# Kernel tuning notes

Hardware: AMD Instinct MI355X
Metric: run time of the kernel (lower is better)

Reference implementation:

```python
import jax, jax.numpy as jnp
import numpy as np

CH = 256
DQK = CH // 8


def setup_inputs() -> dict:
    key = jax.random.key(0)
    ks = jax.random.split(key, 8)
    B, C, H, W = 4, CH, 64, 64
    x = jax.random.normal(ks[0], (B, C, H, W), dtype=jnp.float32)
    s = 1.0 / np.sqrt(C)
    Wq = jax.random.normal(ks[1], (DQK, C), dtype=jnp.float32) * s
    bq = jnp.zeros((DQK,), dtype=jnp.float32)
    Wk = jax.random.normal(ks[2], (DQK, C), dtype=jnp.float32) * s
    bk = jnp.zeros((DQK,), dtype=jnp.float32)
    Wv = jax.random.normal(ks[3], (C, C), dtype=jnp.float32) * s
    bv = jnp.zeros((C,), dtype=jnp.float32)
    gamma = jnp.zeros((1,), dtype=jnp.float32)
    return {"x": x, "Wq": Wq, "bq": bq, "Wk": Wk, "bk": bk, "Wv": Wv, "bv": bv, "gamma": gamma}


def reference(x, Wq, bq, Wk, bk, Wv, bv, gamma):
    B, C, H, W = x.shape
    N = H * W
    xf = x.reshape(B, C, N)                                   # [B, C, N]
    # 1x1 convs == per-position linear maps over channels
    q = jnp.einsum('dc,bcn->bdn', Wq, xf) + bq[None, :, None]  # [B, D, N]
    k = jnp.einsum('dc,bcn->bdn', Wk, xf) + bk[None, :, None]  # [B, D, N]
    v = jnp.einsum('oc,bcn->bon', Wv, xf) + bv[None, :, None]  # [B, C, N]
    # energy[b,i,j] = <q[:, i], k[:, j]>  (no 1/sqrt(d) scaling, as in source)
    energy = jnp.einsum('bdi,bdj->bij', q, k)                  # [B, N, N]
    attn = jax.nn.softmax(energy, axis=-1)                     # softmax over j
    # out[b,c,i] = sum_j v[b,c,j] * attn[b,i,j]
    out = jnp.einsum('bcj,bij->bci', v, attn)                  # [B, C, N]
    return x + gamma[0] * out.reshape(B, C, H, W)
```

## Files before the change

kernel.cpp:

```cpp
#include <hip/hip_runtime.h>
#include <hip/hip_bf16.h>

#define NB   4
#define NC   256
#define NPOS 4096
#define NDQK 32

typedef __bf16 bf16x8  __attribute__((ext_vector_type(8)));
typedef float  f32x16  __attribute__((ext_vector_type(16)));
typedef unsigned int u32x4 __attribute__((ext_vector_type(4)));


__global__ __launch_bounds__(256) void proj_kernel(
    const float* __restrict__ x,
    const float* __restrict__ Wq, const float* __restrict__ bq,
    const float* __restrict__ Wk, const float* __restrict__ bk,
    const float* __restrict__ Wv, const float* __restrict__ bv,
    __hip_bfloat16* __restrict__ Qb, __hip_bfloat16* __restrict__ Kb,
    __hip_bfloat16* __restrict__ Vb)
{
    const int t   = threadIdx.x;
    const int l   = t & 63;
    const int w   = t >> 6;
    const int hi  = l >> 5;
    const int col = l & 31;
    const int row = l & 31;

    const int item = blockIdx.x * 4 + w;
    const int th   = item & 1;
    const int nch  = (item >> 1) & 63;
    const int rest = item >> 7;
    const int g    = rest % 5;
    const int b    = rest / 5;

    const float *W0, *W1, *bs0, *bs1;
    int o0 = 0, o1 = 0;
    if (g < 4) {
        o0 = g * 64; o1 = g * 64 + 32;
        W0 = Wv + (size_t)o0 * NC; W1 = Wv + (size_t)o1 * NC;
        bs0 = bv + o0; bs1 = bv + o1;
    } else {
        W0 = Wq; W1 = Wk; bs0 = bq; bs1 = bk;
    }

    bf16x8 wf0[16], wf1[16];
    const float* Wr0 = W0 + (size_t)row * NC + 8 * hi;
    const float* Wr1 = W1 + (size_t)row * NC + 8 * hi;
    #pragma unroll
    for (int kk = 0; kk < 16; ++kk) {
        float4 a0 = *reinterpret_cast<const float4*>(Wr0 + kk * 16);
        float4 c0 = *reinterpret_cast<const float4*>(Wr0 + kk * 16 + 4);
        float4 a1 = *reinterpret_cast<const float4*>(Wr1 + kk * 16);
        float4 c1 = *reinterpret_cast<const float4*>(Wr1 + kk * 16 + 4);
        bf16x8 f0, f1;
        f0[0] = (__bf16)a0.x; f0[1] = (__bf16)a0.y; f0[2] = (__bf16)a0.z; f0[3] = (__bf16)a0.w;
        f0[4] = (__bf16)c0.x; f0[5] = (__bf16)c0.y; f0[6] = (__bf16)c0.z; f0[7] = (__bf16)c0.w;
        f1[0] = (__bf16)a1.x; f1[1] = (__bf16)a1.y; f1[2] = (__bf16)a1.z; f1[3] = (__bf16)a1.w;
        f1[4] = (__bf16)c1.x; f1[5] = (__bf16)c1.y; f1[6] = (__bf16)c1.z; f1[7] = (__bf16)c1.w;
        wf0[kk] = f0; wf1[kk] = f1;
    }

    const int n0 = nch * 64 + th * 32;
    f32x16 acc0, acc1;
    #pragma unroll
    for (int r = 0; r < 16; ++r) { acc0[r] = 0.f; acc1[r] = 0.f; }

    const float* xcol = x + (size_t)b * NC * NPOS + n0 + col;
    #pragma unroll
    for (int kk = 0; kk < 16; ++kk) {
        bf16x8 bf;
        #pragma unroll
        for (int i = 0; i < 8; ++i)
            bf[i] = (__bf16)xcol[(size_t)(kk * 16 + 8 * hi + i) * NPOS];
        acc0 = __builtin_amdgcn_mfma_f32_32x32x16_bf16(wf0[kk], bf, acc0, 0, 0, 0);
        acc1 = __builtin_amdgcn_mfma_f32_32x32x16_bf16(wf1[kk], bf, acc1, 0, 0, 0);
    }

    if (g < 4) {
        __hip_bfloat16* vt = Vb + (size_t)b * NC * NPOS
                                + (size_t)(n0 >> 5) * 8192 + (size_t)g * 2048
                                + ((col >> 4) << 9) + (((col >> 3) & 1) << 8)
                                + (col & 7);
        #pragma unroll
        for (int r = 0; r < 16; ++r) {
            const int orow = (r & 3) + 8 * (r >> 2) + 4 * hi;
            vt[orow * 8]        = __float2bfloat16(acc0[r] + bs0[orow]);
            vt[1024 + orow * 8] = __float2bfloat16(acc1[r] + bs1[orow]);
        }
    } else {
        #pragma unroll
        for (int r = 0; r < 16; ++r) {
            const int orow = (r & 3) + 8 * (r >> 2) + 4 * hi;
            const size_t nidx = (size_t)(b * NPOS) + n0 + col;
            Qb[nidx * NDQK + orow] =
                __float2bfloat16((acc0[r] + bs0[orow]) * 1.44269504088896f);
            Kb[nidx * NDQK + orow] =
                __float2bfloat16(acc1[r] + bs1[orow]);
        }
    }
}

__global__ __launch_bounds__(512, 2) void attn_kernel(
    const __hip_bfloat16* __restrict__ Qb,
    const __hip_bfloat16* __restrict__ Kb,
    const __hip_bfloat16* __restrict__ Vb,
    const float* __restrict__ x,
    const float* __restrict__ gamma,
    float* __restrict__ out)
{
    __shared__ float olds[NC * 64];
    __shared__ float lsum[64];
    const int t   = threadIdx.x;
    const int l   = t & 63;
    const int w   = t >> 6;
    const int cg  = w & 3;
    const int jh  = w >> 2;
    const int hi  = l >> 5;
    const int q   = l & 31;
    const int bx  = blockIdx.x;
    const int b   = (bx >> 1) & 3;
    const int qt  = ((bx >> 3) << 1) | (bx & 1);
    const int q0  = qt * 64;
    const int c0w = cg * 64;

    const __bf16* Qp = reinterpret_cast<const __bf16*>(Qb) + (size_t)b * NPOS * NDQK;
    const __bf16* Kp = reinterpret_cast<const __bf16*>(Kb) + (size_t)b * NPOS * NDQK;
    const __bf16* Vp = reinterpret_cast<const __bf16*>(Vb) + (size_t)b * NC * NPOS;

    const int perm = (q & 0x13) | ((q & 4) << 1) | ((q & 8) >> 1);

    const bf16x8 qf00 = *reinterpret_cast<const bf16x8*>(Qp + (size_t)(q0 + q) * NDQK + 8 * hi);
    const bf16x8 qf01 = *reinterpret_cast<const bf16x8*>(Qp + (size_t)(q0 + q) * NDQK + 16 + 8 * hi);
    const bf16x8 qf10 = *reinterpret_cast<const bf16x8*>(Qp + (size_t)(q0 + 32 + q) * NDQK + 8 * hi);
    const bf16x8 qf11 = *reinterpret_cast<const bf16x8*>(Qp + (size_t)(q0 + 32 + q) * NDQK + 16 + 8 * hi);

    const int jt0 = jh * 64;
    const __bf16* kp = Kp + (size_t)perm * NDQK + 8 * hi + (size_t)jt0 * 1024;
    const __bf16* vp = Vp + (size_t)cg * 2048 + l * 8 + (size_t)jt0 * 8192;

    #define LOADT(k0, k1, v0, v1, v2, v3, kptr, vptr)                      \
        asm volatile(                                                      \
            "global_load_dwordx4 %0, %6, off\n\t"                          \
            "global_load_dwordx4 %1, %6, off offset:32\n\t"                \
            "global_load_dwordx4 %2, %7, off\n\t"                          \
            "global_load_dwordx4 %3, %7, off offset:1024\n\t"              \
            "global_load_dwordx4 %4, %7, off offset:2048\n\t"              \
            "global_load_dwordx4 %5, %7, off offset:3072"                  \
            : "=&v"(k0), "=&v"(k1), "=&v"(v0), "=&v"(v1), "=&v"(v2), "=&v"(v3) \
            : "v"(kptr), "v"(vptr)                                         \
            : "memory")

    f32x16 acc00, acc01, acc10, acc11;
    #pragma unroll
    for (int r = 0; r < 16; ++r) { acc00[r] = 0.f; acc01[r] = 0.f; acc10[r] = 0.f; acc11[r] = 0.f; }
    float lp0 = 0.f, lp1 = 0.f;

    f32x16 z16;
    #pragma unroll
    for (int r = 0; r < 16; ++r) z16[r] = 0.f;

    auto compute = [&](u32x4 k0r, u32x4 k1r, u32x4 v0r, u32x4 v1r,
                       u32x4 v2r, u32x4 v3r) {
        const bf16x8 kc0 = __builtin_bit_cast(bf16x8, k0r);
        const bf16x8 kc1 = __builtin_bit_cast(bf16x8, k1r);
        const bf16x8 vc0 = __builtin_bit_cast(bf16x8, v0r);
        const bf16x8 vc1 = __builtin_bit_cast(bf16x8, v1r);
        const bf16x8 vc2 = __builtin_bit_cast(bf16x8, v2r);
        const bf16x8 vc3 = __builtin_bit_cast(bf16x8, v3r);

        f32x16 s0 = __builtin_amdgcn_mfma_f32_32x32x16_bf16(kc0, qf00, z16, 0, 0, 0);
        s0 = __builtin_amdgcn_mfma_f32_32x32x16_bf16(kc1, qf01, s0, 0, 0, 0);
        f32x16 s1 = __builtin_amdgcn_mfma_f32_32x32x16_bf16(kc0, qf10, z16, 0, 0, 0);
        s1 = __builtin_amdgcn_mfma_f32_32x32x16_bf16(kc1, qf11, s1, 0, 0, 0);

        float p0[16], p1[16];
        #pragma unroll
        for (int r = 0; r < 16; ++r) p0[r] = __builtin_amdgcn_exp2f(s0[r]);
        #pragma unroll
        for (int r = 0; r < 16; ++r) p1[r] = __builtin_amdgcn_exp2f(s1[r]);

        lp0 += (((p0[0] + p0[1]) + (p0[2] + p0[3])) + ((p0[4] + p0[5]) + (p0[6] + p0[7])))
             + (((p0[8] + p0[9]) + (p0[10] + p0[11])) + ((p0[12] + p0[13]) + (p0[14] + p0[15])));
        lp1 += (((p1[0] + p1[1]) + (p1[2] + p1[3])) + ((p1[4] + p1[5]) + (p1[6] + p1[7])))
             + (((p1[8] + p1[9]) + (p1[10] + p1[11])) + ((p1[12] + p1[13]) + (p1[14] + p1[15])));

        bf16x8 pa00, pa01, pa10, pa11;
        #pragma unroll
        for (int i = 0; i < 8; ++i) {
            pa00[i] = (__bf16)p0[i]; pa01[i] = (__bf16)p0[8 + i];
            pa10[i] = (__bf16)p1[i]; pa11[i] = (__bf16)p1[8 + i];
        }

        acc00 = __builtin_amdgcn_mfma_f32_32x32x16_bf16(vc0, pa00, acc00, 0, 0, 0);
        acc00 = __builtin_amdgcn_mfma_f32_32x32x16_bf16(vc1, pa01, acc00, 0, 0, 0);
        acc01 = __builtin_amdgcn_mfma_f32_32x32x16_bf16(vc2, pa00, acc01, 0, 0, 0);
        acc01 = __builtin_amdgcn_mfma_f32_32x32x16_bf16(vc3, pa01, acc01, 0, 0, 0);
        acc10 = __builtin_amdgcn_mfma_f32_32x32x16_bf16(vc0, pa10, acc10, 0, 0, 0);
        acc10 = __builtin_amdgcn_mfma_f32_32x32x16_bf16(vc1, pa11, acc10, 0, 0, 0);
        acc11 = __builtin_amdgcn_mfma_f32_32x32x16_bf16(vc2, pa10, acc11, 0, 0, 0);
        acc11 = __builtin_amdgcn_mfma_f32_32x32x16_bf16(vc3, pa11, acc11, 0, 0, 0);
    };

    u32x4 ka0, ka1, va0, va1, va2, va3;
    u32x4 kb0, kb1, vb0, vb1, vb2, vb3;

    LOADT(ka0, ka1, va0, va1, va2, va3, kp, vp);
    kp += 1024; vp += 8192;
    asm volatile("s_waitcnt vmcnt(0)" ::: "memory");
    __builtin_amdgcn_sched_barrier(0);

    #pragma unroll 1
    for (int i = 0; i < 64; i += 2) {
        LOADT(kb0, kb1, vb0, vb1, vb2, vb3, kp, vp);
        __builtin_amdgcn_sched_barrier(0);
        if (i < 62) { kp += 1024; vp += 8192; }
        compute(ka0, ka1, va0, va1, va2, va3);
        asm volatile("s_waitcnt vmcnt(0)" ::: "memory");
        __builtin_amdgcn_sched_barrier(0);

        LOADT(ka0, ka1, va0, va1, va2, va3, kp, vp);
        __builtin_amdgcn_sched_barrier(0);
        if (i < 60) { kp += 1024; vp += 8192; }
        compute(kb0, kb1, vb0, vb1, vb2, vb3);
        asm volatile("s_waitcnt vmcnt(0)" ::: "memory");
        __builtin_amdgcn_sched_barrier(0);
    }
    #undef LOADT

    const float lt0 = lp0 + __shfl_xor(lp0, 32);
    const float lt1 = lp1 + __shfl_xor(lp1, 32);

    if (jh == 0) {
        #pragma unroll
        for (int r = 0; r < 16; ++r) {
            const int crow = (r & 3) + 8 * (r >> 2) + 4 * hi;
            olds[(c0w + crow) * 64 + q]           = acc00[r];
            olds[(c0w + 32 + crow) * 64 + q]      = acc01[r];
            olds[(c0w + crow) * 64 + 32 + q]      = acc10[r];
            olds[(c0w + 32 + crow) * 64 + 32 + q] = acc11[r];
        }
        if (cg == 0) { lsum[q + 32 * hi] = hi ? lt1 : lt0; }
    }
    __syncthreads();
    if (jh == 1) {
        const float gm  = gamma[0];
        const float gl0 = gm / (lt0 + lsum[q]);
        const float gl1 = gm / (lt1 + lsum[32 + q]);
        #pragma unroll
        for (int r = 0; r < 16; ++r) {
            const int crow = (r & 3) + 8 * (r >> 2) + 4 * hi;
            const size_t g00 = ((size_t)(b * NC + c0w + crow)) * NPOS + q0 + q;
            const size_t g01 = g00 + (size_t)32 * NPOS;
            out[g00]      = x[g00]      + gl0 * (acc00[r] + olds[(c0w + crow) * 64 + q]);
            out[g01]      = x[g01]      + gl0 * (acc01[r] + olds[(c0w + 32 + crow) * 64 + q]);
            out[g00 + 32] = x[g00 + 32] + gl1 * (acc10[r] + olds[(c0w + crow) * 64 + 32 + q]);
            out[g01 + 32] = x[g01 + 32] + gl1 * (acc11[r] + olds[(c0w + 32 + crow) * 64 + 32 + q]);
        }
    }
}

extern "C" void kernel_launch(void* const* d_in, const int* in_sizes, int n_in,
                              void* d_out, int out_size, void* d_ws, size_t ws_size,
                              hipStream_t stream) {
    (void)in_sizes; (void)n_in; (void)out_size; (void)ws_size;
    const float* x     = (const float*)d_in[0];
    const float* Wq    = (const float*)d_in[1];
    const float* bq    = (const float*)d_in[2];
    const float* Wk    = (const float*)d_in[3];
    const float* bk    = (const float*)d_in[4];
    const float* Wv    = (const float*)d_in[5];
    const float* bv    = (const float*)d_in[6];
    const float* gamma = (const float*)d_in[7];
    float* out = (float*)d_out;

    char* ws = (char*)d_ws;
    __hip_bfloat16* Qb = (__hip_bfloat16*)(ws);
    __hip_bfloat16* Kb = (__hip_bfloat16*)(ws + (1u << 20));
    __hip_bfloat16* Vb = (__hip_bfloat16*)(ws + (2u << 20));

    proj_kernel<<<640, 256, 0, stream>>>(x, Wq, bq, Wk, bk, Wv, bv, Qb, Kb, Vb);
    attn_kernel<<<256, 512, 0, stream>>>(Qb, Kb, Vb, x, gamma, out);
}
```

Baseline: 96.87 us.

## Split attention blocks by channel group and reduce four key quarters in LDS

Measured after the change: 96.38 us. Within noise of the previous version (-0.5%).

```diff
diff --git a/kernel.cpp b/kernel.cpp
--- a/kernel.cpp
+++ b/kernel.cpp
@@ -100,7 +100,7 @@
     }
 }
 
-__global__ __launch_bounds__(512, 2) void attn_kernel(
+__global__ __launch_bounds__(256, 2) void attn_kernel(
     const __hip_bfloat16* __restrict__ Qb,
     const __hip_bfloat16* __restrict__ Kb,
     const __hip_bfloat16* __restrict__ Vb,
@@ -108,20 +108,20 @@
     const float* __restrict__ gamma,
     float* __restrict__ out)
 {
-    __shared__ float olds[NC * 64];
-    __shared__ float lsum[64];
+    __shared__ float olds[2 * 64 * 64];
+    __shared__ float lsum[4 * 64];
     const int t   = threadIdx.x;
     const int l   = t & 63;
-    const int w   = t >> 6;
-    const int cg  = w & 3;
-    const int jh  = w >> 2;
+    const int jq  = t >> 6;
     const int hi  = l >> 5;
     const int q   = l & 31;
     const int bx  = blockIdx.x;
     const int b   = (bx >> 1) & 3;
-    const int qt  = ((bx >> 3) << 1) | (bx & 1);
+    const int id  = ((bx >> 3) << 1) | (bx & 1);
+    const int qt  = id >> 2;
+    const int cg  = id & 3;
     const int q0  = qt * 64;
-    const int c0w = cg * 64;
+    const int c0  = cg * 64;
 
     const __bf16* Qp = reinterpret_cast<const __bf16*>(Qb) + (size_t)b * NPOS * NDQK;
     const __bf16* Kp = reinterpret_cast<const __bf16*>(Kb) + (size_t)b * NPOS * NDQK;
@@ -134,7 +134,7 @@
     const bf16x8 qf10 = *reinterpret_cast<const bf16x8*>(Qp + (size_t)(q0 + 32 + q) * NDQK + 8 * hi);
     const bf16x8 qf11 = *reinterpret_cast<const bf16x8*>(Qp + (size_t)(q0 + 32 + q) * NDQK + 16 + 8 * hi);
 
-    const int jt0 = jh * 64;
+    const int jt0 = jq * 32;
     const __bf16* kp = Kp + (size_t)perm * NDQK + 8 * hi + (size_t)jt0 * 1024;
     const __bf16* vp = Vp + (size_t)cg * 2048 + l * 8 + (size_t)jt0 * 8192;
 
@@ -210,17 +210,17 @@
     __builtin_amdgcn_sched_barrier(0);
 
     #pragma unroll 1
-    for (int i = 0; i < 64; i += 2) {
+    for (int i = 0; i < 32; i += 2) {
         LOADT(kb0, kb1, vb0, vb1, vb2, vb3, kp, vp);
         __builtin_amdgcn_sched_barrier(0);
-        if (i < 62) { kp += 1024; vp += 8192; }
+        if (i < 30) { kp += 1024; vp += 8192; }
         compute(ka0, ka1, va0, va1, va2, va3);
         asm volatile("s_waitcnt vmcnt(0)" ::: "memory");
         __builtin_amdgcn_sched_barrier(0);
 
         LOADT(ka0, ka1, va0, va1, va2, va3, kp, vp);
         __builtin_amdgcn_sched_barrier(0);
-        if (i < 60) { kp += 1024; vp += 8192; }
+        if (i < 30) { kp += 1024; vp += 8192; }
         compute(kb0, kb1, vb0, vb1, vb2, vb3);
         asm volatile("s_waitcnt vmcnt(0)" ::: "memory");
         __builtin_amdgcn_sched_barrier(0);
@@ -230,31 +230,41 @@
     const float lt0 = lp0 + __shfl_xor(lp0, 32);
     const float lt1 = lp1 + __shfl_xor(lp1, 32);
 
-    if (jh == 0) {
+    lsum[jq * 64 + 32 * hi + q] = hi ? lt1 : lt0;
+
+    float* buf = olds + (jq & 1) * 4096;
+    if (jq < 2) {
         #pragma unroll
         for (int r = 0; r < 16; ++r) {
             const int crow = (r & 3) + 8 * (r >> 2) + 4 * hi;
-            olds[(c0w + crow) * 64 + q]           = acc00[r];
-            olds[(c0w + 32 + crow) * 64 + q]      = acc01[r];
-            olds[(c0w + crow) * 64 + 32 + q]      = acc10[r];
-            olds[(c0w + 32 + crow) * 64 + 32 + q] = acc11[r];
-        }
-        if (cg == 0) { lsum[q + 32 * hi] = hi ? lt1 : lt0; }
+            buf[(crow) * 64 + q]           = acc00[r];
+            buf[(32 + crow) * 64 + q]      = acc01[r];
+            buf[(crow) * 64 + 32 + q]      = acc10[r];
+            buf[(32 + crow) * 64 + 32 + q] = acc11[r];
+        }
     }
     __syncthreads();
-    if (jh == 1) {
-        const float gm  = gamma[0];
-        const float gl0 = gm / (lt0 + lsum[q]);
-        const float gl1 = gm / (lt1 + lsum[32 + q]);
+    if (jq >= 2) {
         #pragma unroll
         for (int r = 0; r < 16; ++r) {
             const int crow = (r & 3) + 8 * (r >> 2) + 4 * hi;
-            const size_t g00 = ((size_t)(b * NC + c0w + crow)) * NPOS + q0 + q;
-            const size_t g01 = g00 + (size_t)32 * NPOS;
-            out[g00]      = x[g00]      + gl0 * (acc00[r] + olds[(c0w + crow) * 64 + q]);
-            out[g01]      = x[g01]      + gl0 * (acc01[r] + olds[(c0w + 32 + crow) * 64 + q]);
-            out[g00 + 32] = x[g00 + 32] + gl1 * (acc10[r] + olds[(c0w + crow) * 64 + 32 + q]);
-            out[g01 + 32] = x[g01 + 32] + gl1 * (acc11[r] + olds[(c0w + 32 + crow) * 64 + 32 + q]);
+            buf[(crow) * 64 + q]           += acc00[r];
+            buf[(32 + crow) * 64 + q]      += acc01[r];
+            buf[(crow) * 64 + 32 + q]      += acc10[r];
+            buf[(32 + crow) * 64 + 32 + q] += acc11[r];
+        }
+    }
+    __syncthreads();
+    {
+        const float gm   = gamma[0];
+        const float ltot = lsum[l] + lsum[64 + l] + lsum[128 + l] + lsum[192 + l];
+        const float gl   = gm / ltot;
+        #pragma unroll
+        for (int rr = 0; rr < 16; ++rr) {
+            const int c = jq * 16 + rr;
+            const float v = olds[c * 64 + l] + olds[4096 + c * 64 + l];
+            const size_t gi = ((size_t)(b * NC + c0 + c)) * NPOS + q0 + l;
+            out[gi] = x[gi] + gl * v;
         }
     }
 }
@@ -279,5 +289,5 @@
     __hip_bfloat16* Vb = (__hip_bfloat16*)(ws + (2u << 20));
 
     proj_kernel<<<640, 256, 0, stream>>>(x, Wq, bq, Wk, bk, Wv, bv, Qb, Kb, Vb);
-    attn_kernel<<<256, 512, 0, stream>>>(Qb, Kb, Vb, x, gamma, out);
+    attn_kernel<<<1024, 256, 0, stream>>>(Qb, Kb, Vb, x, gamma, out);
 }
```

## Share QK^T softmax work across waves via LDS and DMA K/V tiles

Applied to the files above, without the earlier changes.

Result: faster. 91.97 us (-5.1%).

```diff
diff --git a/kernel.cpp b/kernel.cpp
--- a/kernel.cpp
+++ b/kernel.cpp
@@ -8,7 +8,9 @@
 
 typedef __bf16 bf16x8  __attribute__((ext_vector_type(8)));
 typedef float  f32x16  __attribute__((ext_vector_type(16)));
-typedef unsigned int u32x4 __attribute__((ext_vector_type(4)));
+
+typedef __attribute__((address_space(3))) char*       lds_ptr_t;
+typedef const __attribute__((address_space(1))) char* glb_ptr_t;
 
 
 __global__ __launch_bounds__(256) void proj_kernel(
@@ -91,16 +93,22 @@
         #pragma unroll
         for (int r = 0; r < 16; ++r) {
             const int orow = (r & 3) + 8 * (r >> 2) + 4 * hi;
-            const size_t nidx = (size_t)(b * NPOS) + n0 + col;
-            Qb[nidx * NDQK + orow] =
+            Qb[((size_t)(b * NPOS) + n0 + col) * NDQK + orow] =
                 __float2bfloat16((acc0[r] + bs0[orow]) * 1.44269504088896f);
-            Kb[nidx * NDQK + orow] =
+        }
+        const int prow = (col & 0x13) | ((col & 4) << 1) | ((col & 8) >> 1);
+        __hip_bfloat16* kt = Kb + (size_t)b * (NPOS * 32)
+                                + (size_t)(n0 >> 5) * 1024 + prow * 8;
+        #pragma unroll
+        for (int r = 0; r < 16; ++r) {
+            const int orow = (r & 3) + 8 * (r >> 2) + 4 * hi;
+            kt[(orow >> 4) * 512 + ((orow >> 3) & 1) * 256 + (orow & 7)] =
                 __float2bfloat16(acc1[r] + bs1[orow]);
         }
     }
 }
 
-__global__ __launch_bounds__(512, 2) void attn_kernel(
+__global__ __launch_bounds__(256, 1) void attn_kernel(
     const __hip_bfloat16* __restrict__ Qb,
     const __hip_bfloat16* __restrict__ Kb,
     const __hip_bfloat16* __restrict__ Vb,
@@ -108,47 +116,47 @@
     const float* __restrict__ gamma,
     float* __restrict__ out)
 {
-    __shared__ float olds[NC * 64];
-    __shared__ float lsum[64];
-    const int t   = threadIdx.x;
-    const int l   = t & 63;
-    const int w   = t >> 6;
-    const int cg  = w & 3;
-    const int jh  = w >> 2;
-    const int hi  = l >> 5;
-    const int q   = l & 31;
-    const int bx  = blockIdx.x;
-    const int b   = (bx >> 1) & 3;
-    const int qt  = ((bx >> 3) << 1) | (bx & 1);
-    const int q0  = qt * 64;
-    const int c0w = cg * 64;
+    __shared__ __align__(16) char smem[8192 + 32768 + 16384 + 1024];
+    const int t  = threadIdx.x;
+    const int l  = t & 63;
+    const int w  = t >> 6;
+    const int hi = l >> 5;
+    const int q  = l & 31;
+    const int bx = blockIdx.x;
+    const int b  = (bx >> 1) & 3;
+    const int qt = ((bx >> 3) << 1) | (bx & 1);
+    const int q0 = qt * 64;
+    const int c0 = w * 64;
 
     const __bf16* Qp = reinterpret_cast<const __bf16*>(Qb) + (size_t)b * NPOS * NDQK;
-    const __bf16* Kp = reinterpret_cast<const __bf16*>(Kb) + (size_t)b * NPOS * NDQK;
+    const __bf16* Kp = reinterpret_cast<const __bf16*>(Kb) + (size_t)b * (NPOS * 32);
     const __bf16* Vp = reinterpret_cast<const __bf16*>(Vb) + (size_t)b * NC * NPOS;
-
-    const int perm = (q & 0x13) | ((q & 4) << 1) | ((q & 8) >> 1);
 
     const bf16x8 qf00 = *reinterpret_cast<const bf16x8*>(Qp + (size_t)(q0 + q) * NDQK + 8 * hi);
     const bf16x8 qf01 = *reinterpret_cast<const bf16x8*>(Qp + (size_t)(q0 + q) * NDQK + 16 + 8 * hi);
     const bf16x8 qf10 = *reinterpret_cast<const bf16x8*>(Qp + (size_t)(q0 + 32 + q) * NDQK + 8 * hi);
     const bf16x8 qf11 = *reinterpret_cast<const bf16x8*>(Qp + (size_t)(q0 + 32 + q) * NDQK + 16 + 8 * hi);
-
-    const int jt0 = jh * 64;
-    const __bf16* kp = Kp + (size_t)perm * NDQK + 8 * hi + (size_t)jt0 * 1024;
-    const __bf16* vp = Vp + (size_t)cg * 2048 + l * 8 + (size_t)jt0 * 8192;
-
-    #define LOADT(k0, k1, v0, v1, v2, v3, kptr, vptr)                      \
-        asm volatile(                                                      \
-            "global_load_dwordx4 %0, %6, off\n\t"                          \
-            "global_load_dwordx4 %1, %6, off offset:32\n\t"                \
-            "global_load_dwordx4 %2, %7, off\n\t"                          \
-            "global_load_dwordx4 %3, %7, off offset:1024\n\t"              \
-            "global_load_dwordx4 %4, %7, off offset:2048\n\t"              \
-            "global_load_dwordx4 %5, %7, off offset:3072"                  \
-            : "=&v"(k0), "=&v"(k1), "=&v"(v0), "=&v"(v1), "=&v"(v2), "=&v"(v3) \
-            : "v"(kptr), "v"(vptr)                                         \
-            : "memory")
+    asm volatile("" :: "v"(qf00), "v"(qf01), "v"(qf10), "v"(qf11));
+
+    char* kb_lds = smem + w * 2048;
+    char* vb_lds = smem + 8192 + w * 8192;
+    __bf16* kbuf = reinterpret_cast<__bf16*>(kb_lds);
+    __bf16* vbuf = reinterpret_cast<__bf16*>(vb_lds);
+    __bf16* plds = reinterpret_cast<__bf16*>(smem + 40960);
+    float*  lsum = reinterpret_cast<float*>(smem + 57344);
+
+    const __bf16* ksrc = Kp + (size_t)w * 1024 + l * 8;
+    const __bf16* vsrc = Vp + (size_t)w * 2048 + l * 8;
+
+    #define DMA16(dst, src) __builtin_amdgcn_global_load_lds( \
+        (glb_ptr_t)(const char*)(src), (lds_ptr_t)(dst), 16, 0, 0)
+    #define DMAK(tp) do { DMA16(kb_lds, (tp)); DMA16(kb_lds + 1024, (tp) + 512); } while (0)
+    #define DMAV(bi, tp) do {                                   \
+        DMA16(vb_lds + (bi) * 4096,        (tp));               \
+        DMA16(vb_lds + (bi) * 4096 + 1024, (tp) + 512);         \
+        DMA16(vb_lds + (bi) * 4096 + 2048, (tp) + 1024);        \
+        DMA16(vb_lds + (bi) * 4096 + 3072, (tp) + 1536);        \
+    } while (0)
 
     f32x16 acc00, acc01, acc10, acc11;
     #pragma unroll
@@ -159,38 +167,16 @@
     #pragma unroll
     for (int r = 0; r < 16; ++r) z16[r] = 0.f;
 
-    auto compute = [&](u32x4 k0r, u32x4 k1r, u32x4 v0r, u32x4 v1r,
-                       u32x4 v2r, u32x4 v3r) {
-        const bf16x8 kc0 = __builtin_bit_cast(bf16x8, k0r);
-        const bf16x8 kc1 = __builtin_bit_cast(bf16x8, k1r);
-        const bf16x8 vc0 = __builtin_bit_cast(bf16x8, v0r);
-        const bf16x8 vc1 = __builtin_bit_cast(bf16x8, v1r);
-        const bf16x8 vc2 = __builtin_bit_cast(bf16x8, v2r);
-        const bf16x8 vc3 = __builtin_bit_cast(bf16x8, v3r);
-
-        f32x16 s0 = __builtin_amdgcn_mfma_f32_32x32x16_bf16(kc0, qf00, z16, 0, 0, 0);
-        s0 = __builtin_amdgcn_mfma_f32_32x32x16_bf16(kc1, qf01, s0, 0, 0, 0);
-        f32x16 s1 = __builtin_amdgcn_mfma_f32_32x32x16_bf16(kc0, qf10, z16, 0, 0, 0);
-        s1 = __builtin_amdgcn_mfma_f32_32x32x16_bf16(kc1, qf11, s1, 0, 0, 0);
-
-        float p0[16], p1[16];
-        #pragma unroll
-        for (int r = 0; r < 16; ++r) p0[r] = __builtin_amdgcn_exp2f(s0[r]);
-        #pragma unroll
-        for (int r = 0; r < 16; ++r) p1[r] = __builtin_amdgcn_exp2f(s1[r]);
-
-        lp0 += (((p0[0] + p0[1]) + (p0[2] + p0[3])) + ((p0[4] + p0[5]) + (p0[6] + p0[7])))
-             + (((p0[8] + p0[9]) + (p0[10] + p0[11])) + ((p0[12] + p0[13]) + (p0[14] + p0[15])));
-        lp1 += (((p1[0] + p1[1]) + (p1[2] + p1[3])) + ((p1[4] + p1[5]) + (p1[6] + p1[7])))
-             + (((p1[8] + p1[9]) + (p1[10] + p1[11])) + ((p1[12] + p1[13]) + (p1[14] + p1[15])));
-
-        bf16x8 pa00, pa01, pa10, pa11;
-        #pragma unroll
-        for (int i = 0; i < 8; ++i) {
-            pa00[i] = (__bf16)p0[i]; pa01[i] = (__bf16)p0[8 + i];
-            pa10[i] = (__bf16)p1[i]; pa11[i] = (__bf16)p1[8 + i];
-        }
-
+    auto PV = [&](int tt, const __bf16* vf) {
+        const bf16x8 vc0 = *reinterpret_cast<const bf16x8*>(vf);
+        const bf16x8 vc1 = *reinterpret_cast<const bf16x8*>(vf + 512);
+        const bf16x8 vc2 = *reinterpret_cast<const bf16x8*>(vf + 1024);
+        const bf16x8 vc3 = *reinterpret_cast<const bf16x8*>(vf + 1536);
+        const __bf16* pf = plds + tt * 2048 + l * 8;
+        const bf16x8 pa00 = *reinterpret_cast<const bf16x8*>(pf);
+        const bf16x8 pa01 = *reinterpret_cast<const bf16x8*>(pf + 512);
+        const bf16x8 pa10 = *reinterpret_cast<const bf16x8*>(pf + 1024);
+        const bf16x8 pa11 = *reinterpret_cast<const bf16x8*>(pf + 1536);
         acc00 = __builtin_amdgcn_mfma_f32_32x32x16_bf16(vc0, pa00, acc00, 0, 0, 0);
         acc00 = __builtin_amdgcn_mfma_f32_32x32x16_bf16(vc1, pa01, acc00, 0, 0, 0);
         acc01 = __builtin_amdgcn_mfma_f32_32x32x16_bf16(vc2, pa00, acc01, 0, 0, 0);
@@ -201,61 +187,106 @@
         acc11 = __builtin_amdgcn_mfma_f32_32x32x16_bf16(vc3, pa11, acc11, 0, 0, 0);
     };
 
-    u32x4 ka0, ka1, va0, va1, va2, va3;
-    u32x4 kb0, kb1, vb0, vb1, vb2, vb3;
-
-    LOADT(ka0, ka1, va0, va1, va2, va3, kp, vp);
-    kp += 1024; vp += 8192;
-    asm volatile("s_waitcnt vmcnt(0)" ::: "memory");
-    __builtin_amdgcn_sched_barrier(0);
+    DMAK(ksrc);
+    DMAV(0, vsrc);
 
     #pragma unroll 1
-    for (int i = 0; i < 64; i += 2) {
-        LOADT(kb0, kb1, vb0, vb1, vb2, vb3, kp, vp);
-        __builtin_amdgcn_sched_barrier(0);
-        if (i < 62) { kp += 1024; vp += 8192; }
-        compute(ka0, ka1, va0, va1, va2, va3);
-        asm volatile("s_waitcnt vmcnt(0)" ::: "memory");
-        __builtin_amdgcn_sched_barrier(0);
-
-        LOADT(ka0, ka1, va0, va1, va2, va3, kp, vp);
-        __builtin_amdgcn_sched_barrier(0);
-        if (i < 60) { kp += 1024; vp += 8192; }
-        compute(kb0, kb1, vb0, vb1, vb2, vb3);
-        asm volatile("s_waitcnt vmcnt(0)" ::: "memory");
-        __builtin_amdgcn_sched_barrier(0);
-    }
-    #undef LOADT
+    for (int r = 0; r < 32; ++r) {
+        asm volatile("s_waitcnt vmcnt(4)" ::: "memory");
+        __builtin_amdgcn_sched_barrier(0);
+        {
+            const bf16x8 kc0 = *reinterpret_cast<const bf16x8*>(kbuf + l * 8);
+            const bf16x8 kc1 = *reinterpret_cast<const bf16x8*>(kbuf + 512 + l * 8);
+            f32x16 s0 = __builtin_amdgcn_mfma_f32_32x32x16_bf16(kc0, qf00, z16, 0, 0, 0);
+            s0 = __builtin_amdgcn_mfma_f32_32x32x16_bf16(kc1, qf01, s0, 0, 0, 0);
+            f32x16 s1 = __builtin_amdgcn_mfma_f32_32x32x16_bf16(kc0, qf10, z16, 0, 0, 0);
+            s1 = __builtin_amdgcn_mfma_f32_32x32x16_bf16(kc1, qf11, s1, 0, 0, 0);
+
+            float p0[16], p1[16];
+            #pragma unroll
+            for (int i = 0; i < 16; ++i) p0[i] = __builtin_amdgcn_exp2f(s0[i]);
+            #pragma unroll
+            for (int i = 0; i < 16; ++i) p1[i] = __builtin_amdgcn_exp2f(s1[i]);
+
+            lp0 += (((p0[0] + p0[1]) + (p0[2] + p0[3])) + ((p0[4] + p0[5]) + (p0[6] + p0[7])))
+                 + (((p0[8] + p0[9]) + (p0[10] + p0[11])) + ((p0[12] + p0[13]) + (p0[14] + p0[15])));
+            lp1 += (((p1[0] + p1[1]) + (p1[2] + p1[3])) + ((p1[4] + p1[5]) + (p1[6] + p1[7])))
+                 + (((p1[8] + p1[9]) + (p1[10] + p1[11])) + ((p1[12] + p1[13]) + (p1[14] + p1[15])));
+
+            bf16x8 pa00, pa01, pa10, pa11;
+            #pragma unroll
+            for (int i = 0; i < 8; ++i) {
+                pa00[i] = (__bf16)p0[i]; pa01[i] = (__bf16)p0[8 + i];
+                pa10[i] = (__bf16)p1[i]; pa11[i] = (__bf16)p1[8 + i];
+            }
+            __bf16* pw = plds + w * 2048 + l * 8;
+            *reinterpret_cast<bf16x8*>(pw)        = pa00;
+            *reinterpret_cast<bf16x8*>(pw + 512)  = pa01;
+            *reinterpret_cast<bf16x8*>(pw + 1024) = pa10;
+            *reinterpret_cast<bf16x8*>(pw + 1536) = pa11;
+        }
+        asm volatile("s_waitcnt lgkmcnt(0)" ::: "memory");
+        __builtin_amdgcn_s_barrier();
+        __builtin_amdgcn_sched_barrier(0);
+
+        DMAV(1, vsrc + 1 * 8192);
+        asm volatile("s_waitcnt vmcnt(4)" ::: "memory");
+        __builtin_amdgcn_sched_barrier(0);
+        PV(0, vbuf + l * 8);
+
+        asm volatile("s_waitcnt lgkmcnt(0)" ::: "memory");
+        __builtin_amdgcn_sched_barrier(0);
+        DMAV(0, vsrc + 2 * 8192);
+        asm volatile("s_waitcnt vmcnt(4)" ::: "memory");
+        __builtin_amdgcn_sched_barrier(0);
+        PV(1, vbuf + 2048 + l * 8);
+
+        asm volatile("s_waitcnt lgkmcnt(0)" ::: "memory");
+        __builtin_amdgcn_sched_barrier(0);
+        DMAV(1, vsrc + 3 * 8192);
+        asm volatile("s_waitcnt vmcnt(4)" ::: "memory");
+        __builtin_amdgcn_sched_barrier(0);
+        PV(2, vbuf + l * 8);
+
+        asm volatile("s_waitcnt lgkmcnt(0)" ::: "memory");
+        __builtin_amdgcn_sched_barrier(0);
+        ksrc += 4096;
+        vsrc += 4 * 8192;
+        if (r < 31) {
+            DMAK(ksrc);
+            DMAV(0, vsrc);
+            asm volatile("s_waitcnt vmcnt(6)" ::: "memory");
+        } else {
+            asm volatile("s_waitcnt vmcnt(0)" ::: "memory");
+        }
+        __builtin_amdgcn_sched_barrier(0);
+        PV(3, vbuf + 2048 + l * 8);
+
+        asm volatile("s_waitcnt lgkmcnt(0)" ::: "memory");
+        __builtin_amdgcn_s_barrier();
+        __builtin_amdgcn_sched_barrier(0);
+    }
+    #undef DMA16
+    #undef DMAK
+    #undef DMAV
 
     const float lt0 = lp0 + __shfl_xor(lp0, 32);
     const float lt1 = lp1 + __shfl_xor(lp1, 32);
-
-    if (jh == 0) {
-        #pragma unroll
-        for (int r = 0; r < 16; ++r) {
-            const int crow = (r & 3) + 8 * (r >> 2) + 4 * hi;
-            olds[(c0w + crow) * 64 + q]           = acc00[r];
-            olds[(c0w + 32 + crow) * 64 + q]      = acc01[r];
-            olds[(c0w + crow) * 64 + 32 + q]      = acc10[r];
-            olds[(c0w + 32 + crow) * 64 + 32 + q] = acc11[r];
-        }
-        if (cg == 0) { lsum[q + 32 * hi] = hi ? lt1 : lt0; }
-    }
+    lsum[w * 64 + 32 * hi + q] = hi ? lt1 : lt0;
     __syncthreads();
-    if (jh == 1) {
-        const float gm  = gamma[0];
-        const float gl0 = gm / (lt0 + lsum[q]);
-        const float gl1 = gm / (lt1 + lsum[32 + q]);
-        #pragma unroll
-        for (int r = 0; r < 16; ++r) {
-            const int crow = (r & 3) + 8 * (r >> 2) + 4 * hi;
-            const size_t g00 = ((size_t)(b * NC + c0w + crow)) * NPOS + q0 + q;
-            const size_t g01 = g00 + (size_t)32 * NPOS;
-            out[g00]      = x[g00]      + gl0 * (acc00[r] + olds[(c0w + crow) * 64 + q]);
-            out[g01]      = x[g01]      + gl0 * (acc01[r] + olds[(c0w + 32 + crow) * 64 + q]);
-            out[g00 + 32] = x[g00 + 32] + gl1 * (acc10[r] + olds[(c0w + crow) * 64 + 32 + q]);
-            out[g01 + 32] = x[g01 + 32] + gl1 * (acc11[r] + olds[(c0w + 32 + crow) * 64 + 32 + q]);
-        }
+
+    const float gm  = gamma[0];
+    const float gl0 = gm / (lsum[q]      + lsum[64 + q]  + lsum[128 + q] + lsum[192 + q]);
+    const float gl1 = gm / (lsum[32 + q] + lsum[96 + q]  + lsum[160 + q] + lsum[224 + q]);
+    #pragma unroll
+    for (int r = 0; r < 16; ++r) {
+        const int crow = (r & 3) + 8 * (r >> 2) + 4 * hi;
+        const size_t g00 = ((size_t)(b * NC + c0 + crow)) * NPOS + q0 + q;
+        const size_t g01 = g00 + (size_t)32 * NPOS;
+        out[g00]      = x[g00]      + gl0 * acc00[r];
+        out[g01]      = x[g01]      + gl0 * acc01[r];
+        out[g00 + 32] = x[g00 + 32] + gl1 * acc10[r];
+        out[g01 + 32] = x[g01 + 32] + gl1 * acc11[r];
     }
 }
 
@@ -279,5 +310,5 @@
     __hip_bfloat16* Vb = (__hip_bfloat16*)(ws + (2u << 20));
 
     proj_kernel<<<640, 256, 0, stream>>>(x, Wq, bq, Wk, bk, Wv, bv, Qb, Kb, Vb);
-    attn_kernel<<<256, 512, 0, stream>>>(Qb, Kb, Vb, x, gamma, out);
+    attn_kernel<<<256, 256, 0, stream>>>(Qb, Kb, Vb, x, gamma, out);
 }
```
